# Kernel tuning notes

Measured on AMD Instinct MI355X. Metric: run time of the kernel, lower is better.

The kernel has to match this reference:

```python
import jax, jax.numpy as jnp
import numpy as np

N = 100000   # nodes
E = 400000   # edges (before self-loops)
G = 4000     # graphs in batch
F_IN = 32    # node_embedding
HID = 128    # hidden_channels
H = 3        # heads (hard-coded in module)
W3 = H * HID # 384, post-concat width
NC = 10      # num_classes
NL = 4       # num_layers
NEG_SLOPE = 0.2


def _lin(key, fan_in, fan_out):
    return jax.random.normal(key, (fan_in, fan_out), jnp.float32) * (1.0 / np.sqrt(fan_in))


def setup_inputs() -> dict:
    key = jax.random.key(0)
    ks = iter(jax.random.split(key, 40))
    x = jax.random.normal(next(ks), (N, F_IN), jnp.float32)
    edge_index = jax.random.randint(next(ks), (2, E), 0, N, dtype=jnp.int32)
    batch = jnp.sort(jax.random.randint(next(ks), (N,), 0, G, dtype=jnp.int32))
    inp = dict(x=x, edge_index=edge_index, batch=batch)
    # MLP stem
    inp['lin1_w'] = _lin(next(ks), F_IN, 2 * HID); inp['lin1_b'] = jnp.zeros((2 * HID,), jnp.float32)
    inp['lin2_w'] = _lin(next(ks), 2 * HID, HID);  inp['lin2_b'] = jnp.zeros((HID,), jnp.float32)
    # conv1: GATConv(HID -> HID, heads=3)
    inp['w0'] = _lin(next(ks), HID, W3)
    inp['as0'] = jax.random.normal(next(ks), (H, HID), jnp.float32) * 0.1
    inp['ad0'] = jax.random.normal(next(ks), (H, HID), jnp.float32) * 0.1
    inp['b0'] = jnp.zeros((W3,), jnp.float32)
    # remaining NL-1 convs: GATConv(W3 -> HID, heads=3), stacked
    inp['wl'] = jnp.stack([_lin(next(ks), W3, W3) for _ in range(NL - 1)])
    inp['asl'] = jax.random.normal(next(ks), (NL - 1, H, HID), jnp.float32) * 0.1
    inp['adl'] = jax.random.normal(next(ks), (NL - 1, H, HID), jnp.float32) * 0.1
    inp['bl'] = jnp.zeros((NL - 1, W3), jnp.float32)
    # batch norms (NL total, all width W3)
    inp['gamma'] = jnp.ones((NL, W3), jnp.float32)
    inp['beta'] = jnp.zeros((NL, W3), jnp.float32)
    # head
    inp['lin3_w'] = _lin(next(ks), W3, HID); inp['lin3_b'] = jnp.zeros((HID,), jnp.float32)
    inp['lin4_w'] = _lin(next(ks), HID, NC); inp['lin4_b'] = jnp.zeros((NC,), jnp.float32)
    return inp


def _gat(x, W, a_src, a_dst, bias, src, dst):
    # PyG GATConv, concat heads. x: [N, Fin]
    h = (x @ W).reshape(N, H, HID)                       # [N, H, C]
    es = jnp.einsum('nhc,hc->nh', h, a_src)              # [N, H]
    ed = jnp.einsum('nhc,hc->nh', h, a_dst)
    e = jax.nn.leaky_relu(es[src] + ed[dst], NEG_SLOPE)  # [Etot, H]
    m = jax.ops.segment_max(e, dst, num_segments=N)      # segment softmax over incoming edges
    p = jnp.exp(e - m[dst])
    s = jax.ops.segment_sum(p, dst, num_segments=N)
    alpha = p / s[dst]                                   # every node has a self-loop -> s>0
    out = jax.ops.segment_sum(alpha[:, :, None] * h[src], dst, num_segments=N)
    return out.reshape(N, W3) + bias


def _bn(x, g, b):
    mu = x.mean(0)
    var = x.var(0)
    return (x - mu) * jax.lax.rsqrt(var + 1e-5) * g + b


def reference(x, edge_index, batch, lin1_w, lin1_b, lin2_w, lin2_b,
              w0, as0, ad0, b0, wl, asl, adl, bl, gamma, beta,
              lin3_w, lin3_b, lin4_w, lin4_b):
    loop = jnp.arange(N, dtype=edge_index.dtype)
    src = jnp.concatenate([edge_index[0], loop])  # add_self_loops=True (PyG default)
    dst = jnp.concatenate([edge_index[1], loop])
    h = jax.nn.relu(x @ lin1_w + lin1_b)
    h = jax.nn.relu(h @ lin2_w + lin2_b)
    h = _gat(h, w0, as0, ad0, b0, src, dst)
    h = _bn(h, gamma[0], beta[0])
    for i in range(NL - 1):
        h = _gat(h, wl[i], asl[i], adl[i], bl[i], src, dst)
        h = _bn(h, gamma[i + 1], beta[i + 1])
    # global mean pool over graphs
    sums = jax.ops.segment_sum(h, batch, num_segments=G)
    cnt = jax.ops.segment_sum(jnp.ones((N,), h.dtype), batch, num_segments=G)
    g = sums / jnp.maximum(cnt, 1.0)[:, None]
    g = jax.nn.relu(g @ lin3_w + lin3_b)
    logits = g @ lin4_w + lin4_b
    return jax.nn.log_softmax(logits, axis=-1)
```

## Files before the change

kernel.cpp:

```cpp
#include <hip/hip_runtime.h>

#define NN      100000
#define NN2     100096
#define NE      400000
#define ETOT    500000
#define NG      4000
#define W3D     384
#define HIDD    128
#define NCLS    10
#define NSLICE  256

typedef unsigned short u16;
typedef unsigned int   u32;
typedef unsigned long long u64;
typedef __attribute__((ext_vector_type(8))) short short8;
typedef __attribute__((ext_vector_type(4))) float f32x4;

static __device__ __forceinline__ float bf2f(u16 u) {
  return __uint_as_float(((u32)u) << 16);
}
static __device__ __forceinline__ float bflo(u32 u) {
  return __uint_as_float(u << 16);
}
static __device__ __forceinline__ float bfhi(u32 u) {
  return __uint_as_float(u & 0xffff0000u);
}
static __device__ __forceinline__ u16 f2b(float f) {
  u32 u = __float_as_uint(f);
  u32 r = (u + 0x7fffu + ((u >> 16) & 1u)) >> 16;
  return (u16)r;
}

static __device__ __forceinline__ void llds16(const u16* g, u16* l) {
  __builtin_amdgcn_global_load_lds(
      (const __attribute__((address_space(1))) void*)(u64)(const void*)g,
      (__attribute__((address_space(3))) void*)(u64)(void*)l, 16, 0, 0);
}

__global__ void mg_zero_out(float* out, int n) {
  int i = blockIdx.x * 256 + threadIdx.x;
  if (i < n) out[i] = 0.f;
}

__global__ void mg_cvt_x(const float* __restrict__ x, u16* __restrict__ Xb) {
  int idx = blockIdx.x * 256 + threadIdx.x;
  if (idx >= NN2 * 64) return;
  int row = idx >> 6, col = idx & 63;
  Xb[idx] = (row < NN && col < 32) ? f2b(x[row * 32 + col]) : (u16)0;
}

__global__ void mg_transpose_pad(const float* __restrict__ in, u16* __restrict__ out,
                                 int K, int Nn, int Kpad) {
  int idx = blockIdx.x * 256 + threadIdx.x;
  if (idx >= Nn * Kpad) return;
  int n = idx / Kpad, k = idx - n * Kpad;
  out[idx] = (k < K) ? f2b(in[k * Nn + n]) : (u16)0;
}

__global__ void mg_fold_w(const u16* __restrict__ Wt, const float* __restrict__ scale,
                          const float* __restrict__ shift, u16* __restrict__ Wp,
                          float* __restrict__ bp) {
  __shared__ float red[128];
  int j = blockIdx.x, t = threadIdx.x;
  const u16* src = Wt + (size_t)j * W3D;
  u16* dst = Wp + (size_t)j * W3D;
  float acc = 0.f;
  for (int k = t; k < W3D; k += 128) {
    float w = bf2f(src[k]);
    dst[k] = f2b(w * scale[k]);
    acc += w * shift[k];
  }
  red[t] = acc; __syncthreads();
  for (int off = 64; off; off >>= 1) {
    if (t < off) red[t] += red[t + off];
    __syncthreads();
  }
  if (t == 0) bp[j] = red[0];
}

__global__ void mg_edge_histo(const int* __restrict__ ei, int* __restrict__ deg) {
  int e = blockIdx.x * 256 + threadIdx.x;
  if (e >= ETOT) return;
  int d = (e < NE) ? ei[NE + e] : (e - NE);
  atomicAdd(&deg[d], 1);
}

__global__ void mg_scan1(const int* __restrict__ in, int* __restrict__ bsum, int n) {
  __shared__ int sd[256];
  int tid = threadIdx.x;
  int base = blockIdx.x * 1024 + tid * 4;
  int s = 0;
#pragma unroll
  for (int j = 0; j < 4; ++j) { int i = base + j; if (i < n) s += in[i]; }
  sd[tid] = s; __syncthreads();
  for (int off = 128; off > 0; off >>= 1) {
    if (tid < off) sd[tid] += sd[tid + off];
    __syncthreads();
  }
  if (tid == 0) bsum[blockIdx.x] = sd[0];
}

__global__ void mg_scan2(int* __restrict__ bsum, int nb) {
  __shared__ int sd[256];
  int tid = threadIdx.x;
  int v = (tid < nb) ? bsum[tid] : 0;
  sd[tid] = v; __syncthreads();
  for (int off = 1; off < 256; off <<= 1) {
    int t = (tid >= off) ? sd[tid - off] : 0;
    __syncthreads();
    sd[tid] += t;
    __syncthreads();
  }
  if (tid < nb) bsum[tid] = sd[tid] - v;
}

__global__ void mg_scan3(const int* __restrict__ in, const int* __restrict__ bexcl,
                         int* __restrict__ out, int n) {
  __shared__ int sd[256];
  int tid = threadIdx.x;
  int base = blockIdx.x * 1024 + tid * 4;
  int loc[4]; int s = 0;
#pragma unroll
  for (int j = 0; j < 4; ++j) { int i = base + j; loc[j] = (i < n) ? in[i] : 0; s += loc[j]; }
  sd[tid] = s; __syncthreads();
  for (int off = 1; off < 256; off <<= 1) {
    int t = (tid >= off) ? sd[tid - off] : 0;
    __syncthreads();
    sd[tid] += t;
    __syncthreads();
  }
  int run = sd[tid] - s + bexcl[blockIdx.x];
#pragma unroll
  for (int j = 0; j < 4; ++j) {
    int i = base + j;
    if (i < n) { out[i] = run; run += loc[j]; if (i == n - 1) out[n] = run; }
  }
}

__global__ void mg_edge_scatter(const int* __restrict__ ei, int* __restrict__ fill,
                                int* __restrict__ colsrc) {
  int e = blockIdx.x * 256 + threadIdx.x;
  if (e >= ETOT) return;
  int s, d;
  if (e < NE) { s = ei[e]; d = ei[NE + e]; } else { s = e - NE; d = s; }
  int pos = atomicAdd(&fill[d], 1);
  colsrc[pos] = s;
}

__global__ void mg_graph_ptr(const int* __restrict__ batch, int* __restrict__ gptr) {
  int g = blockIdx.x * 256 + threadIdx.x;
  if (g > NG) return;
  if (g == NG) { gptr[NG] = NN; return; }
  int lo = 0, hi = NN;
  while (lo < hi) { int mid = (lo + hi) >> 1; if (batch[mid] < g) lo = mid + 1; else hi = mid; }
  gptr[g] = lo;
}

#define GBM 128
#define GBN 128
#define GBK 32
#define CP  130

__global__ __launch_bounds__(256) void mg_gemm(
    const u16* __restrict__ Ag, const u16* __restrict__ Bt,
    int Mstore, int Nn, int K,
    u16* __restrict__ Cb, const float* __restrict__ bias, int relu,
    const float* __restrict__ asrc, const float* __restrict__ adst,
    float* __restrict__ aes, float* __restrict__ aed) {
  __shared__ u16 lds[17408];
  int tid = threadIdx.x;
  int n0 = blockIdx.x * GBN, m0 = blockIdx.y * GBM;
  int lane = tid & 63, wv = tid >> 6;
  int mw = (wv & 1) * 64, nw = (wv >> 1) * 64;
  int lr = lane & 15, lq = lane >> 4;
  int rr = lane & 15, cc4 = lane >> 4;

  f32x4 acc[4][4];
#pragma unroll
  for (int mi = 0; mi < 4; ++mi)
#pragma unroll
    for (int ni = 0; ni < 4; ++ni) acc[mi][ni] = (f32x4){0.f, 0.f, 0.f, 0.f};

  const u16* aB = Ag + (size_t)m0 * K + cc4 * 8;
  const u16* bB = Bt + (size_t)n0 * K + cc4 * 8;
  int niter = K >> 5;

#pragma unroll
  for (int j = 0; j < 2; ++j) {
    int sg = wv * 2 + j, grow = sg * 16 + rr;
    llds16(aB + (size_t)grow * K, lds + sg * 512);
    llds16(bB + (size_t)grow * K, lds + 8192 + sg * 512);
  }

  for (int it = 0; it < niter; ++it) {
    __syncthreads();
    if (it + 1 < niter) {
      int k0 = (it + 1) * GBK, b = (it + 1) & 1;
#pragma unroll
      for (int j = 0; j < 2; ++j) {
        int sg = wv * 2 + j, grow = sg * 16 + rr;
        llds16(aB + (size_t)grow * K + k0, lds + b * 4096 + sg * 512);
        llds16(bB + (size_t)grow * K + k0, lds + 8192 + b * 4096 + sg * 512);
      }
    }
    const u16* Al = lds + (it & 1) * 4096;
    const u16* Bl = lds + 8192 + (it & 1) * 4096;
    short8 af[4], bfr[4];
#pragma unroll
    for (int mi = 0; mi < 4; ++mi)
      af[mi] = *(const short8*)(Al + ((mw >> 4) + mi) * 512 + lq * 128 + lr * 8);
#pragma unroll
    for (int ni = 0; ni < 4; ++ni)
      bfr[ni] = *(const short8*)(Bl + ((nw >> 4) + ni) * 512 + lq * 128 + lr * 8);
#pragma unroll
    for (int mi = 0; mi < 4; ++mi)
#pragma unroll
      for (int ni = 0; ni < 4; ++ni)
        acc[mi][ni] = __builtin_amdgcn_mfma_f32_16x16x32_bf16(af[mi], bfr[ni], acc[mi][ni], 0, 0, 0);
  }
  __syncthreads();

  float bvv[4];
#pragma unroll
  for (int ni = 0; ni < 4; ++ni)
    bvv[ni] = bias ? bias[n0 + nw + ni * 16 + lr] : 0.f;

#pragma unroll
  for (int mi = 0; mi < 4; ++mi)
#pragma unroll
    for (int ni = 0; ni < 4; ++ni) {
      int cl = nw + ni * 16 + lr;
      int rb = mw + mi * 16 + lq * 4;
#pragma unroll
      for (int r = 0; r < 4; ++r) {
        float v = acc[mi][ni][r] + bvv[ni];
        if (relu) v = fmaxf(v, 0.f);
        lds[(rb + r) * CP + cl] = f2b(v);
      }
    }
  __syncthreads();

  int rowl = tid >> 1, half = (tid & 1) * 64;
  const u16* src = lds + rowl * CP + half;
  uint4 creg[8];
#pragma unroll
  for (int j = 0; j < 8; ++j) creg[j] = *(const uint4*)(src + j * 8);
  u16* gout = Cb + (size_t)(m0 + rowl) * Nn + n0 + half;
#pragma unroll
  for (int j = 0; j < 8; ++j) *(uint4*)(gout + j * 8) = creg[j];

  if (aes) {
    const float* ap = asrc + n0 + half;
    const float* dp = adst + n0 + half;
    float se = 0.f, de = 0.f;
#pragma unroll
    for (int j = 0; j < 8; ++j) {
      float4 a0 = *(const float4*)(ap + j * 8);
      float4 a1 = *(const float4*)(ap + j * 8 + 4);
      float4 d0 = *(const float4*)(dp + j * 8);
      float4 d1 = *(const float4*)(dp + j * 8 + 4);
      uint4 rv = creg[j];
      float v0 = bflo(rv.x), v1 = bfhi(rv.x), v2 = bflo(rv.y), v3 = bfhi(rv.y);
      float v4 = bflo(rv.z), v5 = bfhi(rv.z), v6 = bflo(rv.w), v7 = bfhi(rv.w);
      se += v0 * a0.x + v1 * a0.y + v2 * a0.z + v3 * a0.w
          + v4 * a1.x + v5 * a1.y + v6 * a1.z + v7 * a1.w;
      de += v0 * d0.x + v1 * d0.y + v2 * d0.z + v3 * d0.w
          + v4 * d1.x + v5 * d1.y + v6 * d1.z + v7 * d1.w;
    }
    se += __shfl_xor(se, 1);
    de += __shfl_xor(de, 1);
    int row = m0 + rowl;
    if ((tid & 1) == 0 && row < Mstore) {
      aes[row * 4 + blockIdx.x] = se;
      aed[row * 4 + blockIdx.x] = de;
    }
  }
}

__global__ __launch_bounds__(256) void mg_aggregate(
    const u16* __restrict__ B, const float* __restrict__ es,
    const float* __restrict__ ed, const int* __restrict__ rowptr,
    const int* __restrict__ colsrc, const float* __restrict__ bias,
    u16* __restrict__ A, float* __restrict__ stats) {
  __shared__ float bS[4 * W3D];
  __shared__ float bQ[4 * W3D];
  int wv = threadIdx.x >> 6, lane = threadIdx.x & 63;
  if (lane < 48) {
    int h = lane >> 4;
    int cc = lane * 8;
    float4 bv0 = *(const float4*)(bias + cc);
    float4 bv1 = *(const float4*)(bias + cc + 4);
    float stS[8], stQ[8];
#pragma unroll
    for (int j = 0; j < 8; ++j) { stS[j] = 0.f; stQ[j] = 0.f; }
#pragma unroll
    for (int sub = 0; sub < 2; ++sub) {
      int n = blockIdx.x * 8 + wv * 2 + sub;
      int r0 = rowptr[n], r1 = rowptr[n + 1];
      float4 edv = *(const float4*)(ed + 4 * n);
      float4 esn = *(const float4*)(es + 4 * n);
      float s0 = esn.x + edv.x; s0 = (s0 > 0.f) ? s0 : 0.2f * s0;
      float s1 = esn.y + edv.y; s1 = (s1 > 0.f) ? s1 : 0.2f * s1;
      float s2 = esn.z + edv.z; s2 = (s2 > 0.f) ? s2 : 0.2f * s2;
      float mh  = (h == 0) ? s0 : ((h == 1) ? s1 : s2);
      float edh = (h == 0) ? edv.x : ((h == 1) ? edv.y : edv.z);
      float accv[8];
#pragma unroll
      for (int j = 0; j < 8; ++j) accv[j] = 0.f;
      float ssum = 0.f;
      int sA = __builtin_amdgcn_readfirstlane(colsrc[r0]);
      float4 evA = *(const float4*)(es + 4 * sA);
      uint4  rvA = *(const uint4*)(B + (size_t)sA * W3D + cc);
      float4 evB = evA; uint4 rvB = rvA;
      if (r0 + 1 < r1) {
        int sB = __builtin_amdgcn_readfirstlane(colsrc[r0 + 1]);
        evB = *(const float4*)(es + 4 * sB);
        rvB = *(const uint4*)(B + (size_t)sB * W3D + cc);
      }
      for (int r = r0; r < r1; ++r) {
        float4 ev = evA; uint4 rv = rvA;
        evA = evB; rvA = rvB;
        if (r + 2 < r1) {
          int sC = __builtin_amdgcn_readfirstlane(colsrc[r + 2]);
          evB = *(const float4*)(es + 4 * sC);
          rvB = *(const uint4*)(B + (size_t)sC * W3D + cc);
        }
        float e = ((h == 0) ? ev.x : ((h == 1) ? ev.y : ev.z)) + edh;
        e = (e > 0.f) ? e : 0.2f * e;
        float p = __expf(e - mh);
        ssum += p;
        accv[0] += p * bflo(rv.x); accv[1] += p * bfhi(rv.x);
        accv[2] += p * bflo(rv.y); accv[3] += p * bfhi(rv.y);
        accv[4] += p * bflo(rv.z); accv[5] += p * bfhi(rv.z);
        accv[6] += p * bflo(rv.w); accv[7] += p * bfhi(rv.w);
      }
      float inv = 1.0f / ssum;
      float v[8];
      v[0] = accv[0] * inv + bv0.x; v[1] = accv[1] * inv + bv0.y;
      v[2] = accv[2] * inv + bv0.z; v[3] = accv[3] * inv + bv0.w;
      v[4] = accv[4] * inv + bv1.x; v[5] = accv[5] * inv + bv1.y;
      v[6] = accv[6] * inv + bv1.z; v[7] = accv[7] * inv + bv1.w;
      uint4 st;
      st.x = (u32)f2b(v[0]) | ((u32)f2b(v[1]) << 16);
      st.y = (u32)f2b(v[2]) | ((u32)f2b(v[3]) << 16);
      st.z = (u32)f2b(v[4]) | ((u32)f2b(v[5]) << 16);
      st.w = (u32)f2b(v[6]) | ((u32)f2b(v[7]) << 16);
      *(uint4*)(A + (size_t)n * W3D + cc) = st;
#pragma unroll
      for (int j = 0; j < 8; ++j) { stS[j] += v[j]; stQ[j] += v[j] * v[j]; }
    }
    *(float4*)(bS + wv * W3D + cc)     = (float4){stS[0], stS[1], stS[2], stS[3]};
    *(float4*)(bS + wv * W3D + cc + 4) = (float4){stS[4], stS[5], stS[6], stS[7]};
    *(float4*)(bQ + wv * W3D + cc)     = (float4){stQ[0], stQ[1], stQ[2], stQ[3]};
    *(float4*)(bQ + wv * W3D + cc + 4) = (float4){stQ[4], stQ[5], stQ[6], stQ[7]};
  }
  __syncthreads();
  for (int t = threadIdx.x; t < W3D; t += 256) {
    float s = 0.f, q = 0.f;
#pragma unroll
    for (int w = 0; w < 4; ++w) { s += bS[w * W3D + t]; q += bQ[w * W3D + t]; }
    float* sl = stats + (size_t)(blockIdx.x & (NSLICE - 1)) * 768;
    atomicAdd(&sl[t], s);
    atomicAdd(&sl[W3D + t], q);
  }
}

__global__ void mg_bn_finalize(const float* __restrict__ stats, const float* __restrict__ gamma,
                               const float* __restrict__ beta, float* __restrict__ scale,
                               float* __restrict__ shift) {
  int c = threadIdx.x;
  float s = 0.f, q = 0.f;
  for (int b = 0; b < NSLICE; ++b) { s += stats[b * 768 + c]; q += stats[b * 768 + W3D + c]; }
  const float invN = 1.0f / (float)NN;
  float mu = s * invN;
  float var = fmaxf(q * invN - mu * mu, 0.f);
  float inv = rsqrtf(var + 1e-5f);
  float g = gamma[c], be = beta[c];
  scale[c] = g * inv;
  shift[c] = be - mu * g * inv;
}

__global__ void mg_pool(const u16* __restrict__ A, const float* __restrict__ scale,
                        const float* __restrict__ shift, const int* __restrict__ gptr,
                        float* __restrict__ pooled) {
  int g = blockIdx.x, c = threadIdx.x;
  int r0 = gptr[g], r1 = gptr[g + 1];
  float acc = 0.f;
  for (int n = r0; n < r1; ++n) acc += bf2f(A[(size_t)n * W3D + c]);
  int cnt = r1 - r0;
  float v = (cnt > 0) ? (acc / (float)cnt) * scale[c] + shift[c] : 0.f;
  pooled[g * W3D + c] = v;
}

__global__ void mg_head(const float* __restrict__ pooled, const float* __restrict__ w3,
                        const float* __restrict__ b3, const float* __restrict__ w4,
                        const float* __restrict__ b4, float* __restrict__ out) {
  __shared__ float p[W3D];
  __shared__ float g2[HIDD];
  __shared__ float lg[NCLS];
  int g = blockIdx.x, t = threadIdx.x;
  for (int i = t; i < W3D; i += 128) p[i] = pooled[g * W3D + i];
  __syncthreads();
  float acc = 0.f;
  for (int k = 0; k < W3D; ++k) acc += p[k] * w3[k * HIDD + t];
  g2[t] = fmaxf(acc + b3[t], 0.f);
  __syncthreads();
  if (t < NCLS) {
    float a = 0.f;
    for (int k = 0; k < HIDD; ++k) a += g2[k] * w4[k * NCLS + t];
    lg[t] = a + b4[t];
  }
  __syncthreads();
  if (t < NCLS) {
    float m = -1e30f;
#pragma unroll
    for (int j = 0; j < NCLS; ++j) m = fmaxf(m, lg[j]);
    float se = 0.f;
#pragma unroll
    for (int j = 0; j < NCLS; ++j) se += __expf(lg[j] - m);
    out[g * NCLS + t] = lg[t] - m - __logf(se);
  }
}

extern "C" void kernel_launch(void* const* d_in, const int* in_sizes, int n_in,
                              void* d_out, int out_size, void* d_ws, size_t ws_size,
                              hipStream_t stream) {
  const float* x     = (const float*)d_in[0];
  const int*   ei    = (const int*)d_in[1];
  const int*   batch = (const int*)d_in[2];
  const float* w1    = (const float*)d_in[3];
  const float* b1    = (const float*)d_in[4];
  const float* w2    = (const float*)d_in[5];
  const float* b2    = (const float*)d_in[6];
  const float* w0    = (const float*)d_in[7];
  const float* as0   = (const float*)d_in[8];
  const float* ad0   = (const float*)d_in[9];
  const float* b0    = (const float*)d_in[10];
  const float* wl    = (const float*)d_in[11];
  const float* asl   = (const float*)d_in[12];
  const float* adl   = (const float*)d_in[13];
  const float* bl    = (const float*)d_in[14];
  const float* gamma = (const float*)d_in[15];
  const float* beta  = (const float*)d_in[16];
  const float* w3    = (const float*)d_in[17];
  const float* b3    = (const float*)d_in[18];
  const float* w4    = (const float*)d_in[19];
  const float* b4    = (const float*)d_in[20];
  float* out = (float*)d_out;

  char* w = (char*)d_ws;
  auto alloc = [&](size_t bytes) -> void* {
    void* p = (void*)w;
    w += (bytes + 255) & ~(size_t)255;
    return p;
  };
  u16*   P      = (u16*)alloc((size_t)NN2 * W3D * 2);
  u16*   Q      = (u16*)alloc((size_t)NN2 * W3D * 2);
  float* es     = (float*)alloc((size_t)NN * 4 * 4);
  float* ed     = (float*)alloc((size_t)NN * 4 * 4);
  int*   deg    = (int*)alloc((size_t)NN * 4);
  int*   rowptr = (int*)alloc((size_t)(NN + 1) * 4);
  int*   fill   = (int*)alloc((size_t)NN * 4);
  int*   colsrc = (int*)alloc((size_t)ETOT * 4);
  int*   bsum   = (int*)alloc(256 * 4);
  float* stats  = (float*)alloc((size_t)NSLICE * 768 * 4);
  float* scale  = (float*)alloc(W3D * 4);
  float* shift  = (float*)alloc(W3D * 4);
  float* bprime = (float*)alloc(W3D * 4);
  int*   gptr   = (int*)alloc((size_t)(NG + 1) * 4);
  float* pooled = (float*)alloc((size_t)NG * W3D * 4);
  u16*   W1T    = (u16*)alloc(256 * 64 * 2);
  u16*   W2T    = (u16*)alloc(128 * 256 * 2);
  u16*   W0T    = (u16*)alloc(384 * 128 * 2);
  u16*   WlT    = (u16*)alloc((size_t)3 * 384 * 384 * 2);
  u16*   WpT    = (u16*)alloc((size_t)384 * 384 * 2);
  u16*   Xb     = Q;

  if ((size_t)(w - (char*)d_ws) > ws_size) {
    mg_zero_out<<<(out_size + 255) / 256, 256, 0, stream>>>(out, out_size);
    return;
  }

  mg_cvt_x<<<(NN2 * 64 + 255) / 256, 256, 0, stream>>>(x, Xb);
  mg_transpose_pad<<<(256 * 64 + 255) / 256, 256, 0, stream>>>(w1, W1T, 32, 256, 64);
  mg_transpose_pad<<<(128 * 256 + 255) / 256, 256, 0, stream>>>(w2, W2T, 256, 128, 256);
  mg_transpose_pad<<<(384 * 128 + 255) / 256, 256, 0, stream>>>(w0, W0T, 128, 384, 128);
  for (int i = 0; i < 3; ++i)
    mg_transpose_pad<<<(384 * 384 + 255) / 256, 256, 0, stream>>>(
        wl + (size_t)i * 384 * 384, WlT + (size_t)i * 384 * 384, 384, 384, 384);

  hipMemsetAsync(deg, 0, (size_t)NN * 4, stream);
  mg_edge_histo<<<(ETOT + 255) / 256, 256, 0, stream>>>(ei, deg);
  int nb = (NN + 1023) / 1024;
  mg_scan1<<<nb, 256, 0, stream>>>(deg, bsum, NN);
  mg_scan2<<<1, 256, 0, stream>>>(bsum, nb);
  mg_scan3<<<nb, 256, 0, stream>>>(deg, bsum, rowptr, NN);
  hipMemcpyAsync(fill, rowptr, (size_t)NN * 4, hipMemcpyDeviceToDevice, stream);
  mg_edge_scatter<<<(ETOT + 255) / 256, 256, 0, stream>>>(ei, fill, colsrc);
  mg_graph_ptr<<<(NG + 1 + 255) / 256, 256, 0, stream>>>(batch, gptr);

  dim3 blk(256);
  int mtiles = NN2 / GBM;

  mg_gemm<<<dim3(2, mtiles), blk, 0, stream>>>(Xb, W1T, NN, 256, 64,
                                               P, b1, 1,
                                               nullptr, nullptr, nullptr, nullptr);
  mg_gemm<<<dim3(1, mtiles), blk, 0, stream>>>(P, W2T, NN, 128, 256,
                                               Q, b2, 1,
                                               nullptr, nullptr, nullptr, nullptr);

  for (int i = 0; i < 4; ++i) {
    int K = (i == 0) ? 128 : 384;
    const u16* Bt;
    const float* bi_g = nullptr;
    if (i == 0) {
      Bt = W0T;
    } else {
      mg_fold_w<<<384, 128, 0, stream>>>(WlT + (size_t)(i - 1) * 384 * 384,
                                         scale, shift, WpT, bprime);
      Bt = WpT;
      bi_g = bprime;
    }
    const float* as = (i == 0) ? as0 : (asl + (size_t)(i - 1) * 384);
    const float* ad = (i == 0) ? ad0 : (adl + (size_t)(i - 1) * 384);
    const float* bi = (i == 0) ? b0  : (bl  + (size_t)(i - 1) * 384);
    hipMemsetAsync(stats, 0, (size_t)NSLICE * 768 * 4, stream);
    mg_gemm<<<dim3(3, mtiles), blk, 0, stream>>>(Q, Bt, NN, W3D, K,
                                                 P, bi_g, 0,
                                                 as, ad, es, ed);
    mg_aggregate<<<NN / 8, 256, 0, stream>>>(P, es, ed, rowptr, colsrc, bi, Q, stats);
    mg_bn_finalize<<<1, 384, 0, stream>>>(stats, gamma + (size_t)i * W3D,
                                          beta + (size_t)i * W3D, scale, shift);
  }

  mg_pool<<<NG, 384, 0, stream>>>(Q, scale, shift, gptr, pooled);
  mg_head<<<NG, 128, 0, stream>>>(pooled, w3, b3, w4, b4, out);
}
```

Baseline: 1.113 ms.

## Triple-buffer GEMM LDS pipeline with vmcnt waits and XCD-aware tile remap

```diff
diff --git a/kernel.cpp b/kernel.cpp
--- a/kernel.cpp
+++ b/kernel.cpp
@@ -36,6 +36,10 @@
       (const __attribute__((address_space(1))) void*)(u64)(const void*)g,
       (__attribute__((address_space(3))) void*)(u64)(void*)l, 16, 0, 0);
 }
+
+#define WAITV4() asm volatile("s_waitcnt vmcnt(4)" ::: "memory")
+#define WAITV0() asm volatile("s_waitcnt vmcnt(0)" ::: "memory")
+#define MEMFENCE() asm volatile("" ::: "memory")
 
 __global__ void mg_zero_out(float* out, int n) {
   int i = blockIdx.x * 256 + threadIdx.x;
@@ -167,9 +171,20 @@
     u16* __restrict__ Cb, const float* __restrict__ bias, int relu,
     const float* __restrict__ asrc, const float* __restrict__ adst,
     float* __restrict__ aes, float* __restrict__ aed) {
-  __shared__ u16 lds[17408];
+  __shared__ u16 lds[24576];
   int tid = threadIdx.x;
-  int n0 = blockIdx.x * GBN, m0 = blockIdx.y * GBM;
+
+  int gx = gridDim.x;
+  int nwg = gx * (int)gridDim.y;
+  int lin = blockIdx.y * gx + blockIdx.x;
+  int q = nwg >> 3, r = nwg & 7;
+  int xcd = lin & 7, sidx = lin >> 3;
+  int nlin = (xcd < r) ? (xcd * (q + 1) + sidx)
+                       : (r * (q + 1) + (xcd - r) * q + sidx);
+  int ntile = nlin % gx;
+  int mtile = nlin / gx;
+  int n0 = ntile * GBN, m0 = mtile * GBM;
+
   int lane = tid & 63, wv = tid >> 6;
   int mw = (wv & 1) * 64, nw = (wv >> 1) * 64;
   int lr = lane & 15, lq = lane >> 4;
@@ -185,26 +200,18 @@
   const u16* bB = Bt + (size_t)n0 * K + cc4 * 8;
   int niter = K >> 5;
 
-#pragma unroll
-  for (int j = 0; j < 2; ++j) {
-    int sg = wv * 2 + j, grow = sg * 16 + rr;
-    llds16(aB + (size_t)grow * K, lds + sg * 512);
-    llds16(bB + (size_t)grow * K, lds + 8192 + sg * 512);
-  }
-
-  for (int it = 0; it < niter; ++it) {
-    __syncthreads();
-    if (it + 1 < niter) {
-      int k0 = (it + 1) * GBK, b = (it + 1) & 1;
-#pragma unroll
-      for (int j = 0; j < 2; ++j) {
-        int sg = wv * 2 + j, grow = sg * 16 + rr;
-        llds16(aB + (size_t)grow * K + k0, lds + b * 4096 + sg * 512);
-        llds16(bB + (size_t)grow * K + k0, lds + 8192 + b * 4096 + sg * 512);
-      }
+  auto stage = [&](int s) {
+    int k0 = s * GBK, b = s % 3;
+#pragma unroll
+    for (int j = 0; j < 2; ++j) {
+      int sg = wv * 2 + j, grow = sg * 16 + rr;
+      llds16(aB + (size_t)grow * K + k0, lds + b * 4096 + sg * 512);
+      llds16(bB + (size_t)grow * K + k0, lds + 12288 + b * 4096 + sg * 512);
     }
-    const u16* Al = lds + (it & 1) * 4096;
-    const u16* Bl = lds + 8192 + (it & 1) * 4096;
+  };
+  auto compute = [&](int it) {
+    const u16* Al = lds + (it % 3) * 4096;
+    const u16* Bl = lds + 12288 + (it % 3) * 4096;
     short8 af[4], bfr[4];
 #pragma unroll
     for (int mi = 0; mi < 4; ++mi)
@@ -217,7 +224,23 @@
 #pragma unroll
       for (int ni = 0; ni < 4; ++ni)
         acc[mi][ni] = __builtin_amdgcn_mfma_f32_16x16x32_bf16(af[mi], bfr[ni], acc[mi][ni], 0, 0, 0);
-  }
+  };
+
+  stage(0);
+  stage(1);
+
+  for (int it = 0; it < niter - 1; ++it) {
+    WAITV4();
+    __builtin_amdgcn_s_barrier();
+    MEMFENCE();
+    if (it + 2 < niter) stage(it + 2);
+    compute(it);
+  }
+  WAITV0();
+  __builtin_amdgcn_s_barrier();
+  MEMFENCE();
+  compute(niter - 1);
+
   __syncthreads();
 
   float bvv[4];
@@ -232,10 +255,10 @@
       int cl = nw + ni * 16 + lr;
       int rb = mw + mi * 16 + lq * 4;
 #pragma unroll
-      for (int r = 0; r < 4; ++r) {
-        float v = acc[mi][ni][r] + bvv[ni];
+      for (int r2 = 0; r2 < 4; ++r2) {
+        float v = acc[mi][ni][r2] + bvv[ni];
         if (relu) v = fmaxf(v, 0.f);
-        lds[(rb + r) * CP + cl] = f2b(v);
+        lds[(rb + r2) * CP + cl] = f2b(v);
       }
     }
   __syncthreads();
@@ -271,8 +294,8 @@
     de += __shfl_xor(de, 1);
     int row = m0 + rowl;
     if ((tid & 1) == 0 && row < Mstore) {
-      aes[row * 4 + blockIdx.x] = se;
-      aed[row * 4 + blockIdx.x] = de;
+      aes[row * 4 + ntile] = se;
+      aed[row * 4 + ntile] = de;
     }
   }
 }
```

Measured after the change: 1.098 ms. No clear change (-1.4%).

## Rewrite GEMM as persistent kernel with LDS-resident swizzled weights and direct A loads

Applied to the files above, without the earlier changes.

```diff
diff --git a/kernel.cpp b/kernel.cpp
--- a/kernel.cpp
+++ b/kernel.cpp
@@ -37,6 +37,8 @@
       (__attribute__((address_space(3))) void*)(u64)(void*)l, 16, 0, 0);
 }
 
+#define WAITV0() asm volatile("s_waitcnt vmcnt(0)" ::: "memory")
+
 __global__ void mg_zero_out(float* out, int n) {
   int i = blockIdx.x * 256 + threadIdx.x;
   if (i < n) out[i] = 0.f;
@@ -53,8 +55,9 @@
                                  int K, int Nn, int Kpad) {
   int idx = blockIdx.x * 256 + threadIdx.x;
   if (idx >= Nn * Kpad) return;
-  int n = idx / Kpad, k = idx - n * Kpad;
-  out[idx] = (k < K) ? f2b(in[k * Nn + n]) : (u16)0;
+  int n = idx / Kpad, kp = idx - n * Kpad;
+  int ks = (((kp >> 3) ^ (n & 7)) << 3) | (kp & 7);
+  out[idx] = (ks < K) ? f2b(in[ks * Nn + n]) : (u16)0;
 }
 
 __global__ void mg_fold_w(const u16* __restrict__ Wt, const float* __restrict__ scale,
@@ -65,10 +68,11 @@
   const u16* src = Wt + (size_t)j * W3D;
   u16* dst = Wp + (size_t)j * W3D;
   float acc = 0.f;
-  for (int k = t; k < W3D; k += 128) {
-    float w = bf2f(src[k]);
-    dst[k] = f2b(w * scale[k]);
-    acc += w * shift[k];
+  for (int kp = t; kp < W3D; kp += 128) {
+    int kt = (((kp >> 3) ^ (j & 7)) << 3) | (kp & 7);
+    float w = bf2f(src[kp]);
+    dst[kp] = f2b(w * scale[kt]);
+    acc += w * shift[kt];
   }
   red[t] = acc; __syncthreads();
   for (int off = 64; off; off >>= 1) {
@@ -156,123 +160,148 @@
   gptr[g] = lo;
 }
 
-#define GBM 128
-#define GBN 128
-#define GBK 32
-#define CP  130
-
-__global__ __launch_bounds__(256) void mg_gemm(
+#define CP 130
+
+template<int K>
+__global__ __launch_bounds__(512, 2) void mg_gemm(
     const u16* __restrict__ Ag, const u16* __restrict__ Bt,
-    int Mstore, int Nn, int K,
+    int MT, int Mstore, int Nn,
     u16* __restrict__ Cb, const float* __restrict__ bias, int relu,
     const float* __restrict__ asrc, const float* __restrict__ adst,
     float* __restrict__ aes, float* __restrict__ aed) {
-  __shared__ u16 lds[17408];
+  constexpr int NITER = K / 32;
+  __shared__ u16 lds[128 * K + 8 * 16 * CP];
+  u16* Blds = lds;
   int tid = threadIdx.x;
-  int n0 = blockIdx.x * GBN, m0 = blockIdx.y * GBM;
   int lane = tid & 63, wv = tid >> 6;
-  int mw = (wv & 1) * 64, nw = (wv >> 1) * 64;
+  int nidx = blockIdx.y, n0 = nidx * 128;
   int lr = lane & 15, lq = lane >> 4;
-  int rr = lane & 15, cc4 = lane >> 4;
-
-  f32x4 acc[4][4];
-#pragma unroll
-  for (int mi = 0; mi < 4; ++mi)
-#pragma unroll
-    for (int ni = 0; ni < 4; ++ni) acc[mi][ni] = (f32x4){0.f, 0.f, 0.f, 0.f};
-
-  const u16* aB = Ag + (size_t)m0 * K + cc4 * 8;
-  const u16* bB = Bt + (size_t)n0 * K + cc4 * 8;
-  int niter = K >> 5;
-
-#pragma unroll
-  for (int j = 0; j < 2; ++j) {
-    int sg = wv * 2 + j, grow = sg * 16 + rr;
-    llds16(aB + (size_t)grow * K, lds + sg * 512);
-    llds16(bB + (size_t)grow * K, lds + 8192 + sg * 512);
-  }
-
-  for (int it = 0; it < niter; ++it) {
-    __syncthreads();
-    if (it + 1 < niter) {
-      int k0 = (it + 1) * GBK, b = (it + 1) & 1;
-#pragma unroll
-      for (int j = 0; j < 2; ++j) {
-        int sg = wv * 2 + j, grow = sg * 16 + rr;
-        llds16(aB + (size_t)grow * K + k0, lds + b * 4096 + sg * 512);
-        llds16(bB + (size_t)grow * K + k0, lds + 8192 + b * 4096 + sg * 512);
+
+  const u16* Bg = Bt + (size_t)n0 * K;
+#pragma unroll
+  for (int s = 0; s < K / 32; ++s) {
+    int off = (wv * (K / 32) + s) * 512;
+    llds16(Bg + off + lane * 8, Blds + off);
+  }
+
+  float bvv[8];
+#pragma unroll
+  for (int ni = 0; ni < 8; ++ni)
+    bvv[ni] = bias ? bias[n0 + ni * 16 + lr] : 0.f;
+
+  WAITV0();
+  __syncthreads();
+
+  u16* strip = lds + 128 * K + wv * (16 * CP);
+
+  int t0 = (int)(((long long)blockIdx.x * MT) / gridDim.x);
+  int t1 = (int)(((long long)(blockIdx.x + 1) * MT) / gridDim.x);
+
+  for (int t = t0; t < t1; ++t) {
+    int rowbase = t * 256 + wv * 32;
+    const u16* Arow = Ag + (size_t)(rowbase + lr) * K + lq * 8;
+
+    f32x4 acc[2][8];
+#pragma unroll
+    for (int mi = 0; mi < 2; ++mi)
+#pragma unroll
+      for (int ni = 0; ni < 8; ++ni) acc[mi][ni] = (f32x4){0.f, 0.f, 0.f, 0.f};
+
+    short8 a0[2], a1[2];
+#pragma unroll
+    for (int mi = 0; mi < 2; ++mi)
+      a0[mi] = *(const short8*)(Arow + (size_t)mi * 16 * K);
+
+#pragma unroll
+    for (int it = 0; it < NITER; it += 2) {
+#pragma unroll
+      for (int mi = 0; mi < 2; ++mi)
+        a1[mi] = *(const short8*)(Arow + (size_t)mi * 16 * K + (it + 1) * 32);
+      {
+        short8 bfr[8];
+#pragma unroll
+        for (int ni = 0; ni < 8; ++ni) {
+          int nl = ni * 16 + lr;
+          int c = (it * 4 + lq) ^ (nl & 7);
+          bfr[ni] = *(const short8*)(Blds + nl * K + (c << 3));
+        }
+#pragma unroll
+        for (int mi = 0; mi < 2; ++mi)
+#pragma unroll
+          for (int ni = 0; ni < 8; ++ni)
+            acc[mi][ni] = __builtin_amdgcn_mfma_f32_16x16x32_bf16(a0[mi], bfr[ni], acc[mi][ni], 0, 0, 0);
+      }
+      if (it + 2 < NITER) {
+#pragma unroll
+        for (int mi = 0; mi < 2; ++mi)
+          a0[mi] = *(const short8*)(Arow + (size_t)mi * 16 * K + (it + 2) * 32);
+      }
+      {
+        short8 bfr[8];
+#pragma unroll
+        for (int ni = 0; ni < 8; ++ni) {
+          int nl = ni * 16 + lr;
+          int c = ((it + 1) * 4 + lq) ^ (nl & 7);
+          bfr[ni] = *(const short8*)(Blds + nl * K + (c << 3));
+        }
+#pragma unroll
+        for (int mi = 0; mi < 2; ++mi)
+#pragma unroll
+          for (int ni = 0; ni < 8; ++ni)
+            acc[mi][ni] = __builtin_amdgcn_mfma_f32_16x16x32_bf16(a1[mi], bfr[ni], acc[mi][ni], 0, 0, 0);
       }
     }
-    const u16* Al = lds + (it & 1) * 4096;
-    const u16* Bl = lds + 8192 + (it & 1) * 4096;
-    short8 af[4], bfr[4];
-#pragma unroll
-    for (int mi = 0; mi < 4; ++mi)
-      af[mi] = *(const short8*)(Al + ((mw >> 4) + mi) * 512 + lq * 128 + lr * 8);
-#pragma unroll
-    for (int ni = 0; ni < 4; ++ni)
-      bfr[ni] = *(const short8*)(Bl + ((nw >> 4) + ni) * 512 + lq * 128 + lr * 8);
-#pragma unroll
-    for (int mi = 0; mi < 4; ++mi)
-#pragma unroll
-      for (int ni = 0; ni < 4; ++ni)
-        acc[mi][ni] = __builtin_amdgcn_mfma_f32_16x16x32_bf16(af[mi], bfr[ni], acc[mi][ni], 0, 0, 0);
-  }
-  __syncthreads();
-
-  float bvv[4];
-#pragma unroll
-  for (int ni = 0; ni < 4; ++ni)
-    bvv[ni] = bias ? bias[n0 + nw + ni * 16 + lr] : 0.f;
-
-#pragma unroll
-  for (int mi = 0; mi < 4; ++mi)
-#pragma unroll
-    for (int ni = 0; ni < 4; ++ni) {
-      int cl = nw + ni * 16 + lr;
-      int rb = mw + mi * 16 + lq * 4;
-#pragma unroll
-      for (int r = 0; r < 4; ++r) {
-        float v = acc[mi][ni][r] + bvv[ni];
-        if (relu) v = fmaxf(v, 0.f);
-        lds[(rb + r) * CP + cl] = f2b(v);
-      }
-    }
-  __syncthreads();
-
-  int rowl = tid >> 1, half = (tid & 1) * 64;
-  const u16* src = lds + rowl * CP + half;
-  uint4 creg[8];
-#pragma unroll
-  for (int j = 0; j < 8; ++j) creg[j] = *(const uint4*)(src + j * 8);
-  u16* gout = Cb + (size_t)(m0 + rowl) * Nn + n0 + half;
-#pragma unroll
-  for (int j = 0; j < 8; ++j) *(uint4*)(gout + j * 8) = creg[j];
-
-  if (aes) {
-    const float* ap = asrc + n0 + half;
-    const float* dp = adst + n0 + half;
-    float se = 0.f, de = 0.f;
-#pragma unroll
-    for (int j = 0; j < 8; ++j) {
-      float4 a0 = *(const float4*)(ap + j * 8);
-      float4 a1 = *(const float4*)(ap + j * 8 + 4);
-      float4 d0 = *(const float4*)(dp + j * 8);
-      float4 d1 = *(const float4*)(dp + j * 8 + 4);
-      uint4 rv = creg[j];
-      float v0 = bflo(rv.x), v1 = bfhi(rv.x), v2 = bflo(rv.y), v3 = bfhi(rv.y);
-      float v4 = bflo(rv.z), v5 = bfhi(rv.z), v6 = bflo(rv.w), v7 = bfhi(rv.w);
-      se += v0 * a0.x + v1 * a0.y + v2 * a0.z + v3 * a0.w
-          + v4 * a1.x + v5 * a1.y + v6 * a1.z + v7 * a1.w;
-      de += v0 * d0.x + v1 * d0.y + v2 * d0.z + v3 * d0.w
-          + v4 * d1.x + v5 * d1.y + v6 * d1.z + v7 * d1.w;
-    }
-    se += __shfl_xor(se, 1);
-    de += __shfl_xor(de, 1);
-    int row = m0 + rowl;
-    if ((tid & 1) == 0 && row < Mstore) {
-      aes[row * 4 + blockIdx.x] = se;
-      aed[row * 4 + blockIdx.x] = de;
+
+#pragma unroll
+    for (int mi = 0; mi < 2; ++mi) {
+#pragma unroll
+      for (int ni = 0; ni < 8; ++ni) {
+#pragma unroll
+        for (int r = 0; r < 4; ++r) {
+          float v = acc[mi][ni][r] + bvv[ni];
+          if (relu) v = fmaxf(v, 0.f);
+          strip[(lq * 4 + r) * CP + ni * 16 + lr] = f2b(v);
+        }
+      }
+      int row16 = lane >> 2, cb = lane & 3;
+      const u16* src = strip + row16 * CP + cb * 32;
+      uint4 c0 = *(const uint4*)(src);
+      uint4 c1 = *(const uint4*)(src + 8);
+      uint4 c2 = *(const uint4*)(src + 16);
+      uint4 c3 = *(const uint4*)(src + 24);
+      int mrow = rowbase + mi * 16 + row16;
+      u16* gout = Cb + (size_t)mrow * Nn + n0 + cb * 32;
+      *(uint4*)(gout)      = c0;
+      *(uint4*)(gout + 8)  = c1;
+      *(uint4*)(gout + 16) = c2;
+      *(uint4*)(gout + 24) = c3;
+
+      if (aes) {
+        const float* ap = asrc + n0 + cb * 32;
+        const float* dp = adst + n0 + cb * 32;
+        float se = 0.f, de = 0.f;
+        uint4 cj[4] = {c0, c1, c2, c3};
+#pragma unroll
+        for (int j = 0; j < 4; ++j) {
+          float4 A0 = *(const float4*)(ap + j * 8);
+          float4 A1 = *(const float4*)(ap + j * 8 + 4);
+          float4 D0 = *(const float4*)(dp + j * 8);
+          float4 D1 = *(const float4*)(dp + j * 8 + 4);
+          uint4 rv = cj[j];
+          float v0 = bflo(rv.x), v1 = bfhi(rv.x), v2 = bflo(rv.y), v3 = bfhi(rv.y);
+          float v4 = bflo(rv.z), v5 = bfhi(rv.z), v6 = bflo(rv.w), v7 = bfhi(rv.w);
+          se += v0 * A0.x + v1 * A0.y + v2 * A0.z + v3 * A0.w
+              + v4 * A1.x + v5 * A1.y + v6 * A1.z + v7 * A1.w;
+          de += v0 * D0.x + v1 * D0.y + v2 * D0.z + v3 * D0.w
+              + v4 * D1.x + v5 * D1.y + v6 * D1.z + v7 * D1.w;
+        }
+        se += __shfl_xor(se, 1); se += __shfl_xor(se, 2);
+        de += __shfl_xor(de, 1); de += __shfl_xor(de, 2);
+        if (cb == 0 && mrow < Mstore) {
+          aes[mrow * 4 + nidx] = se;
+          aed[mrow * 4 + nidx] = de;
+        }
+      }
     }
   }
 }
@@ -499,20 +528,19 @@
   mg_edge_scatter<<<(ETOT + 255) / 256, 256, 0, stream>>>(ei, fill, colsrc);
   mg_graph_ptr<<<(NG + 1 + 255) / 256, 256, 0, stream>>>(batch, gptr);
 
-  dim3 blk(256);
-  int mtiles = NN2 / GBM;
-
-  mg_gemm<<<dim3(2, mtiles), blk, 0, stream>>>(Xb, W1T, NN, 256, 64,
-                                               P, b1, 1,
-                                               nullptr, nullptr, nullptr, nullptr);
-  mg_gemm<<<dim3(1, mtiles), blk, 0, stream>>>(P, W2T, NN, 128, 256,
-                                               Q, b2, 1,
-                                               nullptr, nullptr, nullptr, nullptr);
+  dim3 blk(512);
+  const int MT = NN2 / 256;
+
+  mg_gemm<64><<<dim3(128, 2), blk, 0, stream>>>(Xb, W1T, MT, NN, 256,
+                                                P, b1, 1,
+                                                nullptr, nullptr, nullptr, nullptr);
+  mg_gemm<256><<<dim3(256, 1), blk, 0, stream>>>(P, W2T, MT, NN, 128,
+                                                 Q, b2, 1,
+                                                 nullptr, nullptr, nullptr, nullptr);
 
   for (int i = 0; i < 4; ++i) {
-    int K = (i == 0) ? 128 : 384;
+    const float* bi_g = nullptr;
     const u16* Bt;
-    const float* bi_g = nullptr;
     if (i == 0) {
       Bt = W0T;
     } else {
@@ -525,9 +553,14 @@
     const float* ad = (i == 0) ? ad0 : (adl + (size_t)(i - 1) * 384);
     const float* bi = (i == 0) ? b0  : (bl  + (size_t)(i - 1) * 384);
     hipMemsetAsync(stats, 0, (size_t)NSLICE * 768 * 4, stream);
-    mg_gemm<<<dim3(3, mtiles), blk, 0, stream>>>(Q, Bt, NN, W3D, K,
-                                                 P, bi_g, 0,
-                                                 as, ad, es, ed);
+    if (i == 0)
+      mg_gemm<128><<<dim3(85, 3), blk, 0, stream>>>(Q, Bt, MT, NN, W3D,
+                                                    P, bi_g, 0,
+                                                    as, ad, es, ed);
+    else
+      mg_gemm<384><<<dim3(85, 3), blk, 0, stream>>>(Q, Bt, MT, NN, W3D,
+                                                    P, bi_g, 0,
+                                                    as, ad, es, ed);
     mg_aggregate<<<NN / 8, 256, 0, stream>>>(P, es, ed, rowptr, colsrc, bi, Q, stats);
     mg_bn_finalize<<<1, 384, 0, stream>>>(stats, gamma + (size_t)i * W3D,
                                           beta + (size_t)i * W3D, scale, shift);
```

Result: faster. 1.042 ms (-6.4%).
